# Kernel tuning notes

Hardware: AMD Instinct MI355X
Metric: run time of the kernel (lower is better)

Reference implementation:

```python
import jax, jax.numpy as jnp
import numpy as np

B, N, H, IN, OUT = 2, 4096, 64, 32, 8


def setup_inputs() -> dict:
    key = jax.random.key(0)
    ks = jax.random.split(key, 18)
    sc = 0.1  # xavier-ish scale for H=64
    mask = lambda k: (jax.random.uniform(k, (1, N, N)) < 0.1).astype(jnp.float32)
    return {
        "x0": jax.random.normal(ks[0], (B, N, IN), jnp.float32),
        "h0": jax.random.normal(ks[1], (B, N, H), jnp.float32),
        "h1": jax.random.normal(ks[2], (B, N, H), jnp.float32),
        "h2": jax.random.normal(ks[3], (B, N, H), jnp.float32),
        "m00": mask(ks[4]), "m20": mask(ks[5]), "m01": mask(ks[6]),
        "m11": mask(ks[7]), "m12": mask(ks[8]), "m22": mask(ks[9]),
        "Wq": jax.random.normal(ks[10], (3, H, H), jnp.float32) * sc,
        "Wk": jax.random.normal(ks[11], (6, H, H), jnp.float32) * sc,
        "Wsu0": jax.random.normal(ks[12], (H, IN + H), jnp.float32) * sc,
        "Wsu12": jax.random.normal(ks[13], (2, H, H), jnp.float32) * sc,
        "Wdt": jax.random.normal(ks[14], (3, H, H), jnp.float32) * sc,
        "bdt": jnp.zeros((3, H), jnp.float32),
        "step_size": jnp.array(1.0, jnp.float32),
        "out_scale": jnp.array(10.0, jnp.float32),
    }


def _cosine_acc(q, keys_and_masks_and_vals):
    # q: [B,N,H]; each entry: (keys [B,Np,H], mask [1,N,Np], vals [B,Np,H])
    qn = q / jnp.linalg.norm(q, axis=2, keepdims=True)
    acc = 0.0
    for k, m, v in keys_and_masks_and_vals:
        kn = k / jnp.linalg.norm(k, axis=2, keepdims=True)
        scale = 1.0 / jnp.sum(m, axis=2, keepdims=True)
        rel = scale * m * jnp.einsum("bnh,bmh->bnm", qn, kn)  # [B,N,Np]
        acc = acc + jnp.einsum("bnm,bmh->bnh", rel, v)
    return acc


def reference(x0, h0, h1, h2, m00, m20, m01, m11, m12, m22,
              Wq, Wk, Wsu0, Wsu12, Wdt, bdt, step_size, out_scale):
    # queries per successor type, keys per edge; edges (pred->succ):
    # 0->0 (k0), 2->0 (k1), 0->1 (k2), 1->1 (k3), 1->2 (k4), 2->2 (k5)
    q0 = h0 @ Wq[0].T
    q1 = h1 @ Wq[1].T
    q2 = h2 @ Wq[2].T
    acc0 = _cosine_acc(q0, [(h0 @ Wk[0].T, m00, h0), (h2 @ Wk[1].T, m20, h2)])
    acc1 = _cosine_acc(q1, [(h0 @ Wk[2].T, m01, h0), (h1 @ Wk[3].T, m11, h1)])
    acc2 = _cosine_acc(q2, [(h1 @ Wk[4].T, m12, h1), (h2 @ Wk[5].T, m22, h2)])

    def step(h, acc_in, Wsu, t):
        dt = 2.0 * jax.nn.sigmoid(h @ Wdt[t].T + bdt[t]) - 1.0
        return h + step_size * dt * (acc_in @ Wsu.T)

    h0n = step(h0, jnp.concatenate([x0, acc0], axis=2), Wsu0, 0)
    h1n = step(h1, acc1, Wsu12[0], 1)
    h2n = step(h2, acc2, Wsu12[1], 2)
    out2 = out_scale * h2n[:, :, :OUT]
    return (out2, h0n, h1n, h2n)
```

## Files before the change

### kernel.cpp

```cpp
#include <hip/hip_runtime.h>

typedef __bf16 bf16;
typedef bf16 bf16x8 __attribute__((ext_vector_type(8)));
typedef float f32x4 __attribute__((ext_vector_type(4)));
typedef unsigned int uint;
typedef uint u32x4 __attribute__((ext_vector_type(4)));
typedef unsigned short u16x8 __attribute__((ext_vector_type(8)));

constexpr int NT = 4096;

__device__ __forceinline__ bf16x8 ld8f(const float* p) {
    f32x4 a = *(const f32x4*)p;
    f32x4 b = *(const f32x4*)(p + 4);
    bf16x8 v;
    v[0] = (bf16)a[0]; v[1] = (bf16)a[1]; v[2] = (bf16)a[2]; v[3] = (bf16)a[3];
    v[4] = (bf16)b[0]; v[5] = (bf16)b[1]; v[6] = (bf16)b[2]; v[7] = (bf16)b[3];
    return v;
}

__device__ __forceinline__ uint pack2(float a, float b) {
    unsigned short ua = __builtin_bit_cast(unsigned short, (bf16)a);
    unsigned short ub = __builtin_bit_cast(unsigned short, (bf16)b);
    return (uint)ua | ((uint)ub << 16);
}

__global__ __launch_bounds__(256) void prep_kernel(
    const float* __restrict__ h0, const float* __restrict__ h1, const float* __restrict__ h2,
    const float* __restrict__ Wq, const float* __restrict__ Wk,
    bf16* __restrict__ qn, bf16* __restrict__ kn, bf16* __restrict__ vT)
{
    __shared__ __align__(16) unsigned short tlds[4][16][72];
    const int tid = threadIdx.x, wid = tid >> 6, lane = tid & 63;
    const int l15 = lane & 15, quad = lane >> 4;
    const int bx = blockIdx.x;
    const int rt = bx & 127, sl = bx >> 7;
    const int g0 = rt * 64;
    const int grow = g0 + wid * 16 + l15;
    const float* hs[3] = {h0, h1, h2};
    const int predmap[6] = {0, 2, 0, 1, 1, 2};

    if (sl >= 9) {
        const int p = sl - 9;
        bf16x8 af[2];
#pragma unroll
        for (int hc = 0; hc < 2; hc++)
            af[hc] = ld8f(hs[p] + (size_t)grow * 64 + hc * 32 + quad * 8);
#pragma unroll
        for (int hc = 0; hc < 2; hc++)
            *(u16x8*)(&tlds[wid][l15][hc * 32 + quad * 8]) = __builtin_bit_cast(u16x8, af[hc]);
        unsigned short vals[16];
#pragma unroll
        for (int r = 0; r < 16; r++) vals[r] = tlds[wid][r][lane];
        uint us[8];
#pragma unroll
        for (int k = 0; k < 8; k++) us[k] = (uint)vals[2 * k] | ((uint)vals[2 * k + 1] << 16);
        const int gr0 = g0 + wid * 16;
        const int bb = gr0 >> 12, n0 = gr0 & 4095;
        uint* dst = (uint*)(vT + ((size_t)(p * 2 + bb) * 64 + lane) * NT + n0);
        u32x4 w0 = {us[0], us[1], us[2], us[3]};
        u32x4 w1 = {us[4], us[5], us[6], us[7]};
        *(u32x4*)dst = w0;
        *(u32x4*)(dst + 4) = w1;
        return;
    }

    const int pj = sl;
    const float* W = (pj < 3) ? (Wq + pj * 4096) : (Wk + (pj - 3) * 4096);
    const int src = (pj < 3) ? pj : predmap[pj - 3];
    bf16* outp = (pj < 3) ? (qn + (size_t)pj * 2 * NT * 64)
                          : (kn + (size_t)(pj - 3) * 2 * NT * 64);
    bf16x8 af[2];
#pragma unroll
    for (int hc = 0; hc < 2; hc++)
        af[hc] = ld8f(hs[src] + (size_t)grow * 64 + hc * 32 + quad * 8);

    f32x4 s[4];
#pragma unroll
    for (int it = 0; it < 4; it++) {
        f32x4 acc = {0.f, 0.f, 0.f, 0.f};
#pragma unroll
        for (int hc = 0; hc < 2; hc++) {
            bf16x8 wb = ld8f(W + (size_t)(it * 16 + l15) * 64 + hc * 32 + quad * 8);
            acc = __builtin_amdgcn_mfma_f32_16x16x32_bf16(af[hc], wb, acc, 0, 0, 0);
        }
        s[it] = acc;
    }
#pragma unroll
    for (int r = 0; r < 4; r++) {
        float ss = s[0][r] * s[0][r] + s[1][r] * s[1][r] + s[2][r] * s[2][r] + s[3][r] * s[3][r];
        ss += __shfl_xor(ss, 1); ss += __shfl_xor(ss, 2);
        ss += __shfl_xor(ss, 4); ss += __shfl_xor(ss, 8);
        float rn = rsqrtf(ss);
        s[0][r] *= rn; s[1][r] *= rn; s[2][r] *= rn; s[3][r] *= rn;
    }
    const int rowbase = g0 + wid * 16 + quad * 4;
#pragma unroll
    for (int it = 0; it < 4; it++)
#pragma unroll
        for (int r = 0; r < 4; r++)
            outp[(size_t)(rowbase + r) * 64 + it * 16 + l15] = (bf16)s[it][r];
}

template<int JC>
__global__ __launch_bounds__(256, 3) void attn_kernel(
    const bf16* __restrict__ qn, const bf16* __restrict__ kn, const bf16* __restrict__ vT,
    const float* __restrict__ m00, const float* __restrict__ m20, const float* __restrict__ m01,
    const float* __restrict__ m11, const float* __restrict__ m12, const float* __restrict__ m22,
    float* __restrict__ Pacc, float* __restrict__ rsO)
{
    __shared__ __align__(16) bf16 Klds[2][64][72];
    __shared__ __align__(16) bf16 Vlds[2][64][72];
    const int tid = threadIdx.x, wid = tid >> 6, lane = tid & 63;
    const int l15 = lane & 15, quad = lane >> 4;
    const int bx = blockIdx.x;
    const int e = bx / (32 * JC);
    const int rem = bx % (32 * JC);
    const int qt = rem / JC, jcv = rem % JC;
    const int qrow0 = qt * 128, wstrip = wid * 32;
    const int qtypemap[6] = {0, 0, 1, 1, 2, 2};
    const int predmap[6]  = {0, 2, 0, 1, 1, 2};
    const float* masks[6] = {m00, m20, m01, m11, m12, m22};
    const float* __restrict__ mask = masks[e];
    const int qtv = qtypemap[e], pv = predmap[e];
    constexpr int JSPAN = NT / JC;
    constexpr int NI = JSPAN / 64;
    const int jbeg = jcv * JSPAN;

    int s_b[4], s_jl[4], s_ch[4];
#pragma unroll
    for (int i = 0; i < 4; i++) {
        int u = tid + 256 * i;
        s_b[i] = u >> 9; s_jl[i] = (u >> 3) & 63; s_ch[i] = u & 7;
    }

    bf16x8 Qf[2][2][2];
#pragma unroll
    for (int b = 0; b < 2; b++)
#pragma unroll
        for (int mt = 0; mt < 2; mt++)
#pragma unroll
            for (int hc = 0; hc < 2; hc++)
                Qf[b][mt][hc] = *(const bf16x8*)(qn +
                    ((size_t)(qtv * 2 + b) * NT + qrow0 + wstrip + mt * 16 + l15) * 64 +
                    hc * 32 + quad * 8);

    f32x4 acc2[2][4][2];
#pragma unroll
    for (int b = 0; b < 2; b++)
#pragma unroll
        for (int ht = 0; ht < 4; ht++)
#pragma unroll
            for (int mt = 0; mt < 2; mt++) {
                f32x4 z = {0.f, 0.f, 0.f, 0.f};
                acc2[b][ht][mt] = z;
            }
    float rsl[2] = {0.f, 0.f};

    u32x4 kreg[4], vreg[4];
#pragma unroll
    for (int i = 0; i < 4; i++) {
        kreg[i] = *(const u32x4*)(kn + ((size_t)(e * 2 + s_b[i]) * NT + jbeg + s_jl[i]) * 64 + s_ch[i] * 8);
        vreg[i] = *(const u32x4*)(vT + ((size_t)(pv * 2 + s_b[i]) * 64 + s_jl[i]) * NT + jbeg + s_ch[i] * 8);
    }
    f32x4 mv[2][4];
#pragma unroll
    for (int mt = 0; mt < 2; mt++)
#pragma unroll
        for (int jt = 0; jt < 4; jt++)
            mv[mt][jt] = *(const f32x4*)(mask +
                (size_t)(qrow0 + wstrip + mt * 16 + l15) * NT + jbeg + jt * 16 + quad * 4);

#pragma unroll 1
    for (int ji = 0; ji < NI; ji++) {
        const int jn = (ji + 1 < NI) ? (jbeg + (ji + 1) * 64) : jbeg;

        __syncthreads();
#pragma unroll
        for (int i = 0; i < 4; i++) {
            *(u32x4*)(&Klds[s_b[i]][s_jl[i]][s_ch[i] * 8]) = kreg[i];
            *(u32x4*)(&Vlds[s_b[i]][s_jl[i]][s_ch[i] * 8]) = vreg[i];
        }
        __syncthreads();

#pragma unroll
        for (int i = 0; i < 4; i++) {
            kreg[i] = *(const u32x4*)(kn + ((size_t)(e * 2 + s_b[i]) * NT + jn + s_jl[i]) * 64 + s_ch[i] * 8);
            vreg[i] = *(const u32x4*)(vT + ((size_t)(pv * 2 + s_b[i]) * 64 + s_jl[i]) * NT + jn + s_ch[i] * 8);
        }

#pragma unroll
        for (int mt = 0; mt < 2; mt++)
#pragma unroll
            for (int jt = 0; jt < 4; jt++)
                rsl[mt] += mv[mt][jt][0] + mv[mt][jt][1] + mv[mt][jt][2] + mv[mt][jt][3];

        uint Pd[2][4][2][2];
#pragma unroll
        for (int jt = 0; jt < 4; jt++)
#pragma unroll
            for (int b = 0; b < 2; b++) {
                bf16x8 aK0 = *(const bf16x8*)(&Klds[b][jt * 16 + l15][quad * 8]);
                bf16x8 aK1 = *(const bf16x8*)(&Klds[b][jt * 16 + l15][32 + quad * 8]);
#pragma unroll
                for (int mt = 0; mt < 2; mt++) {
                    f32x4 sc = {0.f, 0.f, 0.f, 0.f};
                    sc = __builtin_amdgcn_mfma_f32_16x16x32_bf16(aK0, Qf[b][mt][0], sc, 0, 0, 0);
                    sc = __builtin_amdgcn_mfma_f32_16x16x32_bf16(aK1, Qf[b][mt][1], sc, 0, 0, 0);
                    sc[0] *= mv[mt][jt][0]; sc[1] *= mv[mt][jt][1];
                    sc[2] *= mv[mt][jt][2]; sc[3] *= mv[mt][jt][3];
                    Pd[b][jt][mt][0] = pack2(sc[0], sc[1]);
                    Pd[b][jt][mt][1] = pack2(sc[2], sc[3]);
                }
            }

#pragma unroll
        for (int mt = 0; mt < 2; mt++)
#pragma unroll
            for (int jt = 0; jt < 4; jt++)
                mv[mt][jt] = *(const f32x4*)(mask +
                    (size_t)(qrow0 + wstrip + mt * 16 + l15) * NT + jn + jt * 16 + quad * 4);

#pragma unroll
        for (int b = 0; b < 2; b++) {
            uint Bf[2][2][4];
#pragma unroll
            for (int mt = 0; mt < 2; mt++)
#pragma unroll
                for (int c = 0; c < 2; c++)
#pragma unroll
                    for (int d = 0; d < 2; d++) {
                        uint x = Pd[b][2 * c][mt][d];
                        uint y = Pd[b][2 * c + 1][mt][d];
                        asm("v_permlane32_swap_b32 %0, %1\n\t"
                            "v_permlane16_swap_b32 %0, %1"
                            : "+v"(x), "+v"(y));
                        Bf[mt][c][d]     = x;
                        Bf[mt][c][d + 2] = y;
                    }
#pragma unroll
            for (int ht = 0; ht < 4; ht++)
#pragma unroll
                for (int c = 0; c < 2; c++) {
                    bf16x8 a = *(const bf16x8*)(&Vlds[b][ht * 16 + l15][c * 32 + quad * 8]);
#pragma unroll
                    for (int mt = 0; mt < 2; mt++) {
                        u32x4 t = {Bf[mt][c][0], Bf[mt][c][1], Bf[mt][c][2], Bf[mt][c][3]};
                        bf16x8 bbv = __builtin_bit_cast(bf16x8, t);
                        acc2[b][ht][mt] =
                            __builtin_amdgcn_mfma_f32_16x16x32_bf16(a, bbv, acc2[b][ht][mt], 0, 0, 0);
                    }
                }
        }
    }

#pragma unroll
    for (int b = 0; b < 2; b++)
#pragma unroll
        for (int ht = 0; ht < 4; ht++)
#pragma unroll
            for (int mt = 0; mt < 2; mt++) {
                const int n = qrow0 + wstrip + mt * 16 + l15;
                *(f32x4*)(Pacc + ((((size_t)(jcv * 6 + e) * 2 + b) * NT + n) << 6) +
                          ht * 16 + quad * 4) = acc2[b][ht][mt];
            }
#pragma unroll
    for (int mt = 0; mt < 2; mt++) {
        float v = rsl[mt];
        v += __shfl_xor(v, 16);
        v += __shfl_xor(v, 32);
        if (quad == 0)
            rsO[(size_t)(jcv * 6 + e) * NT + qrow0 + wstrip + mt * 16 + l15] = v;
    }
}

template<int JC>
__global__ __launch_bounds__(256) void update_kernel(
    const float* __restrict__ x0, const float* __restrict__ h0,
    const float* __restrict__ h1, const float* __restrict__ h2,
    const float* __restrict__ Wsu0, const float* __restrict__ Wsu12,
    const float* __restrict__ Wdt, const float* __restrict__ bdt,
    const float* __restrict__ stepp, const float* __restrict__ oscp,
    const float* __restrict__ Pacc, const float* __restrict__ rs,
    float* __restrict__ dout)
{
    const int tid = threadIdx.x, wid = tid >> 6, lane = tid & 63;
    const int l15 = lane & 15, quad = lane >> 4;
    const int bx = blockIdx.x;
    const int rt = bx & 127, t = bx >> 7;
    const int g0 = rt * 64;
    const int grow = g0 + wid * 16 + l15;
    const int n = grow & 4095, bb = grow >> 12;
    const float step = *stepp, osc = *oscp;
    const float* hs[3] = {h0, h1, h2};
    const float* __restrict__ ht_base = hs[t];

    bf16x8 afh[2], afacc[2], afx;
#pragma unroll
    for (int hc = 0; hc < 2; hc++)
        afh[hc] = ld8f(ht_base + (size_t)grow * 64 + hc * 32 + quad * 8);
    if (t == 0) afx = ld8f(x0 + (size_t)grow * 32 + quad * 8);

    float s0 = 0.f, s1 = 0.f;
#pragma unroll
    for (int jc = 0; jc < JC; jc++) {
        s0 += rs[(size_t)(jc * 6 + 2 * t) * NT + n];
        s1 += rs[(size_t)(jc * 6 + 2 * t + 1) * NT + n];
    }
    const float i0 = 1.f / s0, i1 = 1.f / s1;
#pragma unroll
    for (int hc = 0; hc < 2; hc++) {
        f32x4 S0a = {0.f,0.f,0.f,0.f}, S0b = {0.f,0.f,0.f,0.f};
        f32x4 S1a = {0.f,0.f,0.f,0.f}, S1b = {0.f,0.f,0.f,0.f};
#pragma unroll
        for (int jc = 0; jc < JC; jc++) {
            const float* p0 = Pacc + ((((size_t)(jc * 6 + 2 * t) * 2 + bb) * NT + n) << 6) +
                              hc * 32 + quad * 8;
            const float* p1 = Pacc + ((((size_t)(jc * 6 + 2 * t + 1) * 2 + bb) * NT + n) << 6) +
                              hc * 32 + quad * 8;
            S0a += *(const f32x4*)p0;  S0b += *(const f32x4*)(p0 + 4);
            S1a += *(const f32x4*)p1;  S1b += *(const f32x4*)(p1 + 4);
        }
        bf16x8 v;
#pragma unroll
        for (int j = 0; j < 4; j++) v[j]     = (bf16)(S0a[j] * i0 + S1a[j] * i1);
#pragma unroll
        for (int j = 0; j < 4; j++) v[4 + j] = (bf16)(S0b[j] * i0 + S1b[j] * i1);
        afacc[hc] = v;
    }

    float bdtv[4];
#pragma unroll
    for (int it = 0; it < 4; it++)
        bdtv[it] = bdt[t * 64 + it * 16 + l15];

#pragma unroll
    for (int it = 0; it < 4; it++) {
        f32x4 z = {0.f, 0.f, 0.f, 0.f};
        f32x4 u = {0.f, 0.f, 0.f, 0.f};
#pragma unroll
        for (int hc = 0; hc < 2; hc++) {
            bf16x8 wb = ld8f(Wdt + (size_t)t * 4096 + (size_t)(it * 16 + l15) * 64 + hc * 32 + quad * 8);
            z = __builtin_amdgcn_mfma_f32_16x16x32_bf16(afh[hc], wb, z, 0, 0, 0);
        }
        if (t == 0) {
            bf16x8 w0 = ld8f(Wsu0 + (size_t)(it * 16 + l15) * 96 + quad * 8);
            u = __builtin_amdgcn_mfma_f32_16x16x32_bf16(afx, w0, u, 0, 0, 0);
#pragma unroll
            for (int kc = 0; kc < 2; kc++) {
                bf16x8 wk = ld8f(Wsu0 + (size_t)(it * 16 + l15) * 96 + 32 + kc * 32 + quad * 8);
                u = __builtin_amdgcn_mfma_f32_16x16x32_bf16(afacc[kc], wk, u, 0, 0, 0);
            }
        } else {
#pragma unroll
            for (int kc = 0; kc < 2; kc++) {
                bf16x8 wk = ld8f(Wsu12 + (size_t)(t - 1) * 4096 + (size_t)(it * 16 + l15) * 64 + kc * 32 + quad * 8);
                u = __builtin_amdgcn_mfma_f32_16x16x32_bf16(afacc[kc], wk, u, 0, 0, 0);
            }
        }
        const int colg = it * 16 + l15;
#pragma unroll
        for (int r = 0; r < 4; r++) {
            int row = g0 + wid * 16 + quad * 4 + r;
            float zz = z[r] + bdtv[it];
            float dtv = 2.f / (1.f + __expf(-zz)) - 1.f;
            float hval = ht_base[(size_t)row * 64 + colg];
            float hn = hval + step * dtv * u[r];
            dout[65536 + (size_t)t * 524288 + (size_t)row * 64 + colg] = hn;
            if (t == 2 && colg < 8)
                dout[(size_t)row * 8 + colg] = osc * hn;
        }
    }
}

extern "C" void kernel_launch(void* const* d_in, const int* in_sizes, int n_in,
                              void* d_out, int out_size, void* d_ws, size_t ws_size,
                              hipStream_t stream) {
    const float* x0   = (const float*)d_in[0];
    const float* h0   = (const float*)d_in[1];
    const float* h1   = (const float*)d_in[2];
    const float* h2   = (const float*)d_in[3];
    const float* m00  = (const float*)d_in[4];
    const float* m20  = (const float*)d_in[5];
    const float* m01  = (const float*)d_in[6];
    const float* m11  = (const float*)d_in[7];
    const float* m12  = (const float*)d_in[8];
    const float* m22  = (const float*)d_in[9];
    const float* Wq   = (const float*)d_in[10];
    const float* Wk   = (const float*)d_in[11];
    const float* Wsu0 = (const float*)d_in[12];
    const float* Wsu12= (const float*)d_in[13];
    const float* Wdt  = (const float*)d_in[14];
    const float* bdt  = (const float*)d_in[15];
    const float* step = (const float*)d_in[16];
    const float* oscl = (const float*)d_in[17];

    bf16* qn  = (bf16*)d_ws;
    bf16* kn  = qn + 1572864;
    bf16* vT  = kn + 3145728;
    float* Pacc = (float*)(vT + 1572864);

    auto need = [](size_t jc) { return 12582912 + jc * 12582912 + jc * 98304; };
    const int JC = (ws_size >= need(4)) ? 4 : ((ws_size >= need(2)) ? 2 : 1);

    prep_kernel<<<1536, 256, 0, stream>>>(h0, h1, h2, Wq, Wk, qn, kn, vT);

    if (JC == 4) {
        float* rs = Pacc + (size_t)4 * 3145728;
        attn_kernel<4><<<6 * 32 * 4, 256, 0, stream>>>(qn, kn, vT, m00, m20, m01, m11, m12, m22, Pacc, rs);
        update_kernel<4><<<384, 256, 0, stream>>>(x0, h0, h1, h2, Wsu0, Wsu12, Wdt, bdt,
                                                  step, oscl, Pacc, rs, (float*)d_out);
    } else if (JC == 2) {
        float* rs = Pacc + (size_t)2 * 3145728;
        attn_kernel<2><<<6 * 32 * 2, 256, 0, stream>>>(qn, kn, vT, m00, m20, m01, m11, m12, m22, Pacc, rs);
        update_kernel<2><<<384, 256, 0, stream>>>(x0, h0, h1, h2, Wsu0, Wsu12, Wdt, bdt,
                                                  step, oscl, Pacc, rs, (float*)d_out);
    } else {
        float* rs = Pacc + (size_t)1 * 3145728;
        attn_kernel<1><<<6 * 32 * 1, 256, 0, stream>>>(qn, kn, vT, m00, m20, m01, m11, m12, m22, Pacc, rs);
        update_kernel<1><<<384, 256, 0, stream>>>(x0, h0, h1, h2, Wsu0, Wsu12, Wdt, bdt,
                                                  step, oscl, Pacc, rs, (float*)d_out);
    }
}
```

Before: 461.6 us.

## Pack masks into bitmasks in prep and split attention blocks per batch

The prep kernel gains extra blocks that read each float mask once, pack it into a bitmask and compute row counts. The attention kernel then reads compact bits instead of float mask tiles. Previously each attention block streamed the float masks and handled both batches; now each block handles one batch, so the mask is still read per batch but at 1/32 the size. The attention kernel also drops the LDS staging and barriers, reading K and V directly from global memory, and swizzles block order across the XCDs. The costs are an extra mask-pack pass over 400MB of float masks in prep, uncoalesced direct global reads of K/V, and an assumption that mask values are exactly 0 or 1.

Result: slower. 644.8 us (+39.7%).

```diff
diff --git a/kernel.cpp b/kernel.cpp
--- a/kernel.cpp
+++ b/kernel.cpp
@@ -4,6 +4,7 @@
 typedef bf16 bf16x8 __attribute__((ext_vector_type(8)));
 typedef float f32x4 __attribute__((ext_vector_type(4)));
 typedef unsigned int uint;
+typedef uint u32x2 __attribute__((ext_vector_type(2)));
 typedef uint u32x4 __attribute__((ext_vector_type(4)));
 typedef unsigned short u16x8 __attribute__((ext_vector_type(8)));
 
@@ -27,12 +28,43 @@
 __global__ __launch_bounds__(256) void prep_kernel(
     const float* __restrict__ h0, const float* __restrict__ h1, const float* __restrict__ h2,
     const float* __restrict__ Wq, const float* __restrict__ Wk,
-    bf16* __restrict__ qn, bf16* __restrict__ kn, bf16* __restrict__ vT)
+    const float* __restrict__ m00, const float* __restrict__ m20, const float* __restrict__ m01,
+    const float* __restrict__ m11, const float* __restrict__ m12, const float* __restrict__ m22,
+    bf16* __restrict__ qn, bf16* __restrict__ kn, bf16* __restrict__ vT,
+    uint* __restrict__ mb, float* __restrict__ rs2)
 {
     __shared__ __align__(16) unsigned short tlds[4][16][72];
     const int tid = threadIdx.x, wid = tid >> 6, lane = tid & 63;
     const int l15 = lane & 15, quad = lane >> 4;
     const int bx = blockIdx.x;
+
+    if (bx >= 1536) {
+        const int mi = bx - 1536;
+        const int e = mi >> 10, rb = mi & 1023;
+        const int row = rb * 4 + wid;
+        const float* masks[6] = {m00, m20, m01, m11, m12, m22};
+        const float* mrow = masks[e] + (size_t)row * NT + lane * 64;
+        uint lo = 0, hi = 0;
+#pragma unroll
+        for (int k = 0; k < 16; k++) {
+            f32x4 v = *(const f32x4*)(mrow + 4 * k);
+#pragma unroll
+            for (int c = 0; c < 4; c++) {
+                const int idx = 4 * k + c;
+                if (idx < 32) lo |= (v[c] > 0.5f) ? (1u << idx) : 0u;
+                else          hi |= (v[c] > 0.5f) ? (1u << (idx - 32)) : 0u;
+            }
+        }
+        int cnt = __popc(lo) + __popc(hi);
+        cnt += __shfl_xor(cnt, 1);  cnt += __shfl_xor(cnt, 2);
+        cnt += __shfl_xor(cnt, 4);  cnt += __shfl_xor(cnt, 8);
+        cnt += __shfl_xor(cnt, 16); cnt += __shfl_xor(cnt, 32);
+        if (lane == 0) rs2[e * NT + row] = (float)cnt;
+        u32x2 w = {lo, hi};
+        ((u32x2*)(mb + (size_t)(e * NT + row) * 128))[lane] = w;
+        return;
+    }
+
     const int rt = bx & 127, sl = bx >> 7;
     const int g0 = rt * 64;
     const int grow = g0 + wid * 16 + l15;
@@ -102,175 +134,130 @@
 }
 
 template<int JC>
-__global__ __launch_bounds__(256, 3) void attn_kernel(
+__global__ __launch_bounds__(256, 4) void attn_kernel(
     const bf16* __restrict__ qn, const bf16* __restrict__ kn, const bf16* __restrict__ vT,
-    const float* __restrict__ m00, const float* __restrict__ m20, const float* __restrict__ m01,
-    const float* __restrict__ m11, const float* __restrict__ m12, const float* __restrict__ m22,
-    float* __restrict__ Pacc, float* __restrict__ rsO)
+    const uint* __restrict__ mb, float* __restrict__ Pacc)
 {
-    __shared__ __align__(16) bf16 Klds[2][64][72];
-    __shared__ __align__(16) bf16 Vlds[2][64][72];
     const int tid = threadIdx.x, wid = tid >> 6, lane = tid & 63;
     const int l15 = lane & 15, quad = lane >> 4;
-    const int bx = blockIdx.x;
-    const int e = bx / (32 * JC);
-    const int rem = bx % (32 * JC);
-    const int qt = rem / JC, jcv = rem % JC;
-    const int qrow0 = qt * 128, wstrip = wid * 32;
+    constexpr int G = 6 * 32 * 2 * JC;
+    const int bxr = blockIdx.x;
+    const int wg = (bxr & 7) * (G >> 3) + (bxr >> 3);
+    const int jcv = wg % JC;
+    int r = wg / JC;
+    const int b = r & 1; r >>= 1;
+    const int qt = r & 31; const int e = r >> 5;
     const int qtypemap[6] = {0, 0, 1, 1, 2, 2};
     const int predmap[6]  = {0, 2, 0, 1, 1, 2};
-    const float* masks[6] = {m00, m20, m01, m11, m12, m22};
-    const float* __restrict__ mask = masks[e];
     const int qtv = qtypemap[e], pv = predmap[e];
+    const int qrow0 = qt * 128, wstrip = wid * 32;
     constexpr int JSPAN = NT / JC;
     constexpr int NI = JSPAN / 64;
     const int jbeg = jcv * JSPAN;
 
-    int s_b[4], s_jl[4], s_ch[4];
-#pragma unroll
-    for (int i = 0; i < 4; i++) {
-        int u = tid + 256 * i;
-        s_b[i] = u >> 9; s_jl[i] = (u >> 3) & 63; s_ch[i] = u & 7;
-    }
-
-    bf16x8 Qf[2][2][2];
-#pragma unroll
-    for (int b = 0; b < 2; b++)
-#pragma unroll
-        for (int mt = 0; mt < 2; mt++)
-#pragma unroll
-            for (int hc = 0; hc < 2; hc++)
-                Qf[b][mt][hc] = *(const bf16x8*)(qn +
-                    ((size_t)(qtv * 2 + b) * NT + qrow0 + wstrip + mt * 16 + l15) * 64 +
-                    hc * 32 + quad * 8);
-
-    f32x4 acc2[2][4][2];
-#pragma unroll
-    for (int b = 0; b < 2; b++)
-#pragma unroll
-        for (int ht = 0; ht < 4; ht++)
-#pragma unroll
-            for (int mt = 0; mt < 2; mt++) {
-                f32x4 z = {0.f, 0.f, 0.f, 0.f};
-                acc2[b][ht][mt] = z;
-            }
-    float rsl[2] = {0.f, 0.f};
-
-    u32x4 kreg[4], vreg[4];
-#pragma unroll
-    for (int i = 0; i < 4; i++) {
-        kreg[i] = *(const u32x4*)(kn + ((size_t)(e * 2 + s_b[i]) * NT + jbeg + s_jl[i]) * 64 + s_ch[i] * 8);
-        vreg[i] = *(const u32x4*)(vT + ((size_t)(pv * 2 + s_b[i]) * 64 + s_jl[i]) * NT + jbeg + s_ch[i] * 8);
-    }
-    f32x4 mv[2][4];
+    bf16x8 Qf[2][2];
 #pragma unroll
     for (int mt = 0; mt < 2; mt++)
 #pragma unroll
-        for (int jt = 0; jt < 4; jt++)
-            mv[mt][jt] = *(const f32x4*)(mask +
-                (size_t)(qrow0 + wstrip + mt * 16 + l15) * NT + jbeg + jt * 16 + quad * 4);
+        for (int hc = 0; hc < 2; hc++)
+            Qf[mt][hc] = *(const bf16x8*)(qn +
+                ((size_t)(qtv * 2 + b) * NT + qrow0 + wstrip + mt * 16 + l15) * 64 +
+                hc * 32 + quad * 8);
+
+    f32x4 acc2[4][2];
+#pragma unroll
+    for (int ht = 0; ht < 4; ht++)
+#pragma unroll
+        for (int mt = 0; mt < 2; mt++) {
+            f32x4 z = {0.f, 0.f, 0.f, 0.f};
+            acc2[ht][mt] = z;
+        }
+
+    const bf16* Kbase = kn + ((size_t)(e * 2 + b) * NT + jbeg) * 64;
+    const bf16* Vbase = vT + (size_t)(pv * 2 + b) * 64 * NT + jbeg;
+    const uint* mbase[2];
+#pragma unroll
+    for (int mt = 0; mt < 2; mt++)
+        mbase[mt] = mb + (size_t)(e * NT + qrow0 + wstrip + mt * 16 + l15) * 128 + (jbeg >> 5);
+
+    u32x2 mcur[2], mnxt[2];
+#pragma unroll
+    for (int mt = 0; mt < 2; mt++) {
+        mcur[mt] = *(const u32x2*)(mbase[mt]);
+        mnxt[mt] = *(const u32x2*)(mbase[mt] + ((NI > 1) ? 2 : 0));
+    }
 
 #pragma unroll 1
     for (int ji = 0; ji < NI; ji++) {
-        const int jn = (ji + 1 < NI) ? (jbeg + (ji + 1) * 64) : jbeg;
-
-        __syncthreads();
-#pragma unroll
-        for (int i = 0; i < 4; i++) {
-            *(u32x4*)(&Klds[s_b[i]][s_jl[i]][s_ch[i] * 8]) = kreg[i];
-            *(u32x4*)(&Vlds[s_b[i]][s_jl[i]][s_ch[i] * 8]) = vreg[i];
-        }
-        __syncthreads();
-
-#pragma unroll
-        for (int i = 0; i < 4; i++) {
-            kreg[i] = *(const u32x4*)(kn + ((size_t)(e * 2 + s_b[i]) * NT + jn + s_jl[i]) * 64 + s_ch[i] * 8);
-            vreg[i] = *(const u32x4*)(vT + ((size_t)(pv * 2 + s_b[i]) * 64 + s_jl[i]) * NT + jn + s_ch[i] * 8);
-        }
-
+        const int woff2 = (ji + 2 < NI) ? 2 * (ji + 2) : 0;
+        u32x2 mtmp[2];
 #pragma unroll
         for (int mt = 0; mt < 2; mt++)
-#pragma unroll
-            for (int jt = 0; jt < 4; jt++)
-                rsl[mt] += mv[mt][jt][0] + mv[mt][jt][1] + mv[mt][jt][2] + mv[mt][jt][3];
-
-        uint Pd[2][4][2][2];
-#pragma unroll
-        for (int jt = 0; jt < 4; jt++)
-#pragma unroll
-            for (int b = 0; b < 2; b++) {
-                bf16x8 aK0 = *(const bf16x8*)(&Klds[b][jt * 16 + l15][quad * 8]);
-                bf16x8 aK1 = *(const bf16x8*)(&Klds[b][jt * 16 + l15][32 + quad * 8]);
+            mtmp[mt] = *(const u32x2*)(mbase[mt] + woff2);
+
+        const bf16* Kw = Kbase + ji * 64 * 64;
+        uint Pd[4][2][2];
+#pragma unroll
+        for (int jt = 0; jt < 4; jt++) {
+            bf16x8 aK0 = *(const bf16x8*)(Kw + (size_t)(jt * 16 + l15) * 64 + quad * 8);
+            bf16x8 aK1 = *(const bf16x8*)(Kw + (size_t)(jt * 16 + l15) * 64 + 32 + quad * 8);
+#pragma unroll
+            for (int mt = 0; mt < 2; mt++) {
+                f32x4 sc = {0.f, 0.f, 0.f, 0.f};
+                sc = __builtin_amdgcn_mfma_f32_16x16x32_bf16(aK0, Qf[mt][0], sc, 0, 0, 0);
+                sc = __builtin_amdgcn_mfma_f32_16x16x32_bf16(aK1, Qf[mt][1], sc, 0, 0, 0);
+                const uint w = (jt < 2) ? mcur[mt].x : mcur[mt].y;
+                const int sh = (jt & 1) * 16 + quad * 4;
+#pragma unroll
+                for (int k = 0; k < 4; k++)
+                    sc[k] = ((w >> (sh + k)) & 1u) ? sc[k] : 0.0f;
+                Pd[jt][mt][0] = pack2(sc[0], sc[1]);
+                Pd[jt][mt][1] = pack2(sc[2], sc[3]);
+            }
+        }
+#pragma unroll
+        for (int mt = 0; mt < 2; mt++) { mcur[mt] = mnxt[mt]; mnxt[mt] = mtmp[mt]; }
+
+        uint Bf[2][2][4];
+#pragma unroll
+        for (int mt = 0; mt < 2; mt++)
+#pragma unroll
+            for (int c = 0; c < 2; c++)
+#pragma unroll
+                for (int d = 0; d < 2; d++) {
+                    uint x = Pd[2 * c][mt][d];
+                    uint y = Pd[2 * c + 1][mt][d];
+                    asm("v_permlane32_swap_b32 %0, %1\n\t"
+                        "v_permlane16_swap_b32 %0, %1"
+                        : "+v"(x), "+v"(y));
+                    Bf[mt][c][d]     = x;
+                    Bf[mt][c][d + 2] = y;
+                }
+
+        const bf16* Vw = Vbase + ji * 64;
+#pragma unroll
+        for (int ht = 0; ht < 4; ht++)
+#pragma unroll
+            for (int c = 0; c < 2; c++) {
+                bf16x8 a = *(const bf16x8*)(Vw + (size_t)(ht * 16 + l15) * NT + c * 32 + quad * 8);
 #pragma unroll
                 for (int mt = 0; mt < 2; mt++) {
-                    f32x4 sc = {0.f, 0.f, 0.f, 0.f};
-                    sc = __builtin_amdgcn_mfma_f32_16x16x32_bf16(aK0, Qf[b][mt][0], sc, 0, 0, 0);
-                    sc = __builtin_amdgcn_mfma_f32_16x16x32_bf16(aK1, Qf[b][mt][1], sc, 0, 0, 0);
-                    sc[0] *= mv[mt][jt][0]; sc[1] *= mv[mt][jt][1];
-                    sc[2] *= mv[mt][jt][2]; sc[3] *= mv[mt][jt][3];
-                    Pd[b][jt][mt][0] = pack2(sc[0], sc[1]);
-                    Pd[b][jt][mt][1] = pack2(sc[2], sc[3]);
+                    u32x4 t = {Bf[mt][c][0], Bf[mt][c][1], Bf[mt][c][2], Bf[mt][c][3]};
+                    bf16x8 bbv = __builtin_bit_cast(bf16x8, t);
+                    acc2[ht][mt] =
+                        __builtin_amdgcn_mfma_f32_16x16x32_bf16(a, bbv, acc2[ht][mt], 0, 0, 0);
                 }
             }
-
-#pragma unroll
-        for (int mt = 0; mt < 2; mt++)
-#pragma unroll
-            for (int jt = 0; jt < 4; jt++)
-                mv[mt][jt] = *(const f32x4*)(mask +
-                    (size_t)(qrow0 + wstrip + mt * 16 + l15) * NT + jn + jt * 16 + quad * 4);
-
-#pragma unroll
-        for (int b = 0; b < 2; b++) {
-            uint Bf[2][2][4];
-#pragma unroll
-            for (int mt = 0; mt < 2; mt++)
-#pragma unroll
-                for (int c = 0; c < 2; c++)
-#pragma unroll
-                    for (int d = 0; d < 2; d++) {
-                        uint x = Pd[b][2 * c][mt][d];
-                        uint y = Pd[b][2 * c + 1][mt][d];
-                        asm("v_permlane32_swap_b32 %0, %1\n\t"
-                            "v_permlane16_swap_b32 %0, %1"
-                            : "+v"(x), "+v"(y));
-                        Bf[mt][c][d]     = x;
-                        Bf[mt][c][d + 2] = y;
-                    }
-#pragma unroll
-            for (int ht = 0; ht < 4; ht++)
-#pragma unroll
-                for (int c = 0; c < 2; c++) {
-                    bf16x8 a = *(const bf16x8*)(&Vlds[b][ht * 16 + l15][c * 32 + quad * 8]);
-#pragma unroll
-                    for (int mt = 0; mt < 2; mt++) {
-                        u32x4 t = {Bf[mt][c][0], Bf[mt][c][1], Bf[mt][c][2], Bf[mt][c][3]};
-                        bf16x8 bbv = __builtin_bit_cast(bf16x8, t);
-                        acc2[b][ht][mt] =
-                            __builtin_amdgcn_mfma_f32_16x16x32_bf16(a, bbv, acc2[b][ht][mt], 0, 0, 0);
-                    }
-                }
-        }
-    }
-
-#pragma unroll
-    for (int b = 0; b < 2; b++)
-#pragma unroll
-        for (int ht = 0; ht < 4; ht++)
-#pragma unroll
-            for (int mt = 0; mt < 2; mt++) {
-                const int n = qrow0 + wstrip + mt * 16 + l15;
-                *(f32x4*)(Pacc + ((((size_t)(jcv * 6 + e) * 2 + b) * NT + n) << 6) +
-                          ht * 16 + quad * 4) = acc2[b][ht][mt];
-            }
-#pragma unroll
-    for (int mt = 0; mt < 2; mt++) {
-        float v = rsl[mt];
-        v += __shfl_xor(v, 16);
-        v += __shfl_xor(v, 32);
-        if (quad == 0)
-            rsO[(size_t)(jcv * 6 + e) * NT + qrow0 + wstrip + mt * 16 + l15] = v;
-    }
+    }
+
+#pragma unroll
+    for (int ht = 0; ht < 4; ht++)
+#pragma unroll
+        for (int mt = 0; mt < 2; mt++) {
+            const int n = qrow0 + wstrip + mt * 16 + l15;
+            *(f32x4*)(Pacc + ((((size_t)(jcv * 6 + e) * 2 + b) * NT + n) << 6) +
+                      ht * 16 + quad * 4) = acc2[ht][mt];
+        }
 }
 
 template<int JC>
@@ -280,7 +267,7 @@
     const float* __restrict__ Wsu0, const float* __restrict__ Wsu12,
     const float* __restrict__ Wdt, const float* __restrict__ bdt,
     const float* __restrict__ stepp, const float* __restrict__ oscp,
-    const float* __restrict__ Pacc, const float* __restrict__ rs,
+    const float* __restrict__ Pacc, const float* __restrict__ rs2,
     float* __restrict__ dout)
 {
     const int tid = threadIdx.x, wid = tid >> 6, lane = tid & 63;
@@ -300,13 +287,8 @@
         afh[hc] = ld8f(ht_base + (size_t)grow * 64 + hc * 32 + quad * 8);
     if (t == 0) afx = ld8f(x0 + (size_t)grow * 32 + quad * 8);
 
-    float s0 = 0.f, s1 = 0.f;
-#pragma unroll
-    for (int jc = 0; jc < JC; jc++) {
-        s0 += rs[(size_t)(jc * 6 + 2 * t) * NT + n];
-        s1 += rs[(size_t)(jc * 6 + 2 * t + 1) * NT + n];
-    }
-    const float i0 = 1.f / s0, i1 = 1.f / s1;
+    const float i0 = 1.f / rs2[(size_t)(2 * t) * NT + n];
+    const float i1 = 1.f / rs2[(size_t)(2 * t + 1) * NT + n];
 #pragma unroll
     for (int hc = 0; hc < 2; hc++) {
         f32x4 S0a = {0.f,0.f,0.f,0.f}, S0b = {0.f,0.f,0.f,0.f};
@@ -397,27 +379,28 @@
     bf16* qn  = (bf16*)d_ws;
     bf16* kn  = qn + 1572864;
     bf16* vT  = kn + 3145728;
-    float* Pacc = (float*)(vT + 1572864);
-
-    auto need = [](size_t jc) { return 12582912 + jc * 12582912 + jc * 98304; };
+    uint* mb  = (uint*)(vT + 1572864);
+    float* rs2 = (float*)(mb + 3145728);
+    float* Pacc = rs2 + 24576;
+
+    auto need = [](size_t jc) { return 25264128 + jc * 12582912; };
     const int JC = (ws_size >= need(4)) ? 4 : ((ws_size >= need(2)) ? 2 : 1);
 
-    prep_kernel<<<1536, 256, 0, stream>>>(h0, h1, h2, Wq, Wk, qn, kn, vT);
+    prep_kernel<<<7680, 256, 0, stream>>>(h0, h1, h2, Wq, Wk,
+                                          m00, m20, m01, m11, m12, m22,
+                                          qn, kn, vT, mb, rs2);
 
     if (JC == 4) {
-        float* rs = Pacc + (size_t)4 * 3145728;
-        attn_kernel<4><<<6 * 32 * 4, 256, 0, stream>>>(qn, kn, vT, m00, m20, m01, m11, m12, m22, Pacc, rs);
+        attn_kernel<4><<<6 * 32 * 2 * 4, 256, 0, stream>>>(qn, kn, vT, mb, Pacc);
         update_kernel<4><<<384, 256, 0, stream>>>(x0, h0, h1, h2, Wsu0, Wsu12, Wdt, bdt,
-                                                  step, oscl, Pacc, rs, (float*)d_out);
+                                                  step, oscl, Pacc, rs2, (float*)d_out);
     } else if (JC == 2) {
-        float* rs = Pacc + (size_t)2 * 3145728;
-        attn_kernel<2><<<6 * 32 * 2, 256, 0, stream>>>(qn, kn, vT, m00, m20, m01, m11, m12, m22, Pacc, rs);
+        attn_kernel<2><<<6 * 32 * 2 * 2, 256, 0, stream>>>(qn, kn, vT, mb, Pacc);
         update_kernel<2><<<384, 256, 0, stream>>>(x0, h0, h1, h2, Wsu0, Wsu12, Wdt, bdt,
-                                                  step, oscl, Pacc, rs, (float*)d_out);
+                                                  step, oscl, Pacc, rs2, (float*)d_out);
     } else {
-        float* rs = Pacc + (size_t)1 * 3145728;
-        attn_kernel<1><<<6 * 32 * 1, 256, 0, stream>>>(qn, kn, vT, m00, m20, m01, m11, m12, m22, Pacc, rs);
+        attn_kernel<1><<<6 * 32 * 2 * 1, 256, 0, stream>>>(qn, kn, vT, mb, Pacc);
         update_kernel<1><<<384, 256, 0, stream>>>(x0, h0, h1, h2, Wsu0, Wsu12, Wdt, bdt,
-                                                  step, oscl, Pacc, rs, (float*)d_out);
-    }
-}
+                                                  step, oscl, Pacc, rs2, (float*)d_out);
+    }
+}
```
